# Kernel tuning notes

Hardware: AMD Instinct MI355X
Metric: run time of the kernel (lower is better)

Reference implementation:

```python
import jax, jax.numpy as jnp
import numpy as np

FACTOR = 1.0

def _dct_matrix():
    n = 8
    D = np.zeros((n * n, n * n), dtype=np.float32)
    for u in range(n):
        for v in range(n):
            au = 1.0 / np.sqrt(2.0) if u == 0 else 1.0
            av = 1.0 / np.sqrt(2.0) if v == 0 else 1.0
            alpha = au * av * 0.25
            for x in range(n):
                for y in range(n):
                    D[u * n + v, x * n + y] = alpha * np.cos((2 * x + 1) * u * np.pi / 16) * np.cos((2 * y + 1) * v * np.pi / 16)
    return D

def _y_quant_table():
    t = np.array([[16, 11, 10, 16, 24, 40, 51, 61], [12, 12, 14, 19, 26, 58, 60, 55],
                  [14, 13, 16, 24, 40, 57, 69, 56], [14, 17, 22, 29, 51, 87, 80, 62],
                  [18, 22, 37, 56, 68, 109, 103, 77], [24, 35, 55, 64, 81, 104, 113, 92],
                  [49, 64, 78, 87, 103, 121, 120, 101], [72, 92, 95, 98, 112, 100, 103, 99]],
                 dtype=np.float32).T
    return t

def _c_quant_table():
    t = np.full((8, 8), 99, dtype=np.float32)
    t[:4, :4] = np.array([[17, 18, 24, 47], [18, 21, 26, 66], [24, 26, 56, 99], [47, 66, 99, 99]],
                          dtype=np.float32).T
    return t

_D = jnp.asarray(_dct_matrix())          # [64,64]
_QT = jnp.stack([jnp.asarray(_y_quant_table()),
                 jnp.asarray(_c_quant_table()),
                 jnp.asarray(_c_quant_table())], axis=0) * FACTOR  # [3,8,8]

def setup_inputs() -> dict:
    key = jax.random.key(0)
    image = jax.random.uniform(key, (32, 3, 512, 512), dtype=jnp.float32)
    return {"image": image}

def _diffjpeg(image):
    x = jnp.clip(image, 0.0, 1.0)
    B, C, H, W = x.shape  # H, W multiples of 8 -> no padding branch
    r, g, b = x[:, 0], x[:, 1], x[:, 2]
    y = 0.299 * r + 0.587 * g + 0.114 * b
    cb = (b - y) * 0.564 + 0.5
    cr = (r - y) * 0.713 + 0.5
    ycbcr = jnp.stack([y, cb, cr], axis=1)  # [B,3,H,W]
    # blockify into 8x8 tiles
    nh, nw = H // 8, W // 8
    blocks = ycbcr.reshape(B, C, nh, 8, nw, 8).transpose(0, 1, 2, 4, 3, 5)  # [B,C,nh,nw,8,8]
    flat = blocks.reshape(-1, 64) * 255.0 - 128.0
    dct = flat @ _D.T                      # matmul(D, flat.T).T
    dctb = dct.reshape(B, C, nh, nw, 8, 8)
    qte = _QT[None, :, None, None, :, :]   # [1,3,1,1,8,8]
    q = dctb / qte
    q = q + jax.lax.stop_gradient(jnp.round(q) - q)  # STE rounding
    deq = q * qte
    idct = deq.reshape(-1, 64) @ _D        # matmul(D.T, x.T).T
    idct = (idct + 128.0) / 255.0
    img = idct.reshape(B, C, nh, nw, 8, 8).transpose(0, 1, 2, 4, 3, 5).reshape(B, C, H, W)
    yy, ycb, ycr = img[:, 0], img[:, 1] - 0.5, img[:, 2] - 0.5
    rr = yy + 1.403 * ycr
    gg = yy - 0.714 * ycr - 0.344 * ycb
    bb = yy + 1.773 * ycb
    rgb = jnp.clip(jnp.stack([rr, gg, bb], axis=1), 0.0, 1.0)
    return jnp.clip(rgb, 0.0, 1.0)

def reference(image):
    return _diffjpeg(image)
```

## Files before the change

kernel.cpp:

```cpp
#include <hip/hip_runtime.h>

typedef float f32x2 __attribute__((ext_vector_type(2)));

#define K4 0.353553391f
#define K1 0.490392640f
#define K3 0.415734806f
#define K5 0.277785117f
#define K7 0.097545161f
#define K2 0.461939766f
#define K6 0.191341716f

__device__ __align__(16) const float YQT[64] = {
    16.f, 12.f, 14.f, 14.f,  18.f,  24.f,  49.f,  72.f,
    11.f, 12.f, 13.f, 17.f,  22.f,  35.f,  64.f,  92.f,
    10.f, 14.f, 16.f, 22.f,  37.f,  55.f,  78.f,  95.f,
    16.f, 19.f, 24.f, 29.f,  56.f,  64.f,  87.f,  98.f,
    24.f, 26.f, 40.f, 51.f,  68.f,  81.f, 103.f, 112.f,
    40.f, 58.f, 57.f, 87.f, 109.f, 104.f, 121.f, 100.f,
    51.f, 60.f, 69.f, 80.f, 103.f, 113.f, 120.f, 103.f,
    61.f, 55.f, 56.f, 62.f,  77.f,  92.f, 101.f,  99.f
};
__device__ __align__(16) const float RYQT[64] = {
    1.f/16.f, 1.f/12.f, 1.f/14.f, 1.f/14.f, 1.f/18.f,  1.f/24.f,  1.f/49.f,  1.f/72.f,
    1.f/11.f, 1.f/12.f, 1.f/13.f, 1.f/17.f, 1.f/22.f,  1.f/35.f,  1.f/64.f,  1.f/92.f,
    1.f/10.f, 1.f/14.f, 1.f/16.f, 1.f/22.f, 1.f/37.f,  1.f/55.f,  1.f/78.f,  1.f/95.f,
    1.f/16.f, 1.f/19.f, 1.f/24.f, 1.f/29.f, 1.f/56.f,  1.f/64.f,  1.f/87.f,  1.f/98.f,
    1.f/24.f, 1.f/26.f, 1.f/40.f, 1.f/51.f, 1.f/68.f,  1.f/81.f,  1.f/103.f, 1.f/112.f,
    1.f/40.f, 1.f/58.f, 1.f/57.f, 1.f/87.f, 1.f/109.f, 1.f/104.f, 1.f/121.f, 1.f/100.f,
    1.f/51.f, 1.f/60.f, 1.f/69.f, 1.f/80.f, 1.f/103.f, 1.f/113.f, 1.f/120.f, 1.f/103.f,
    1.f/61.f, 1.f/55.f, 1.f/56.f, 1.f/62.f, 1.f/77.f,  1.f/92.f,  1.f/101.f, 1.f/99.f
};
__device__ __align__(16) const float CQ[64] = {
    17.f, 18.f, 24.f, 47.f, 99.f, 99.f, 99.f, 99.f,
    18.f, 21.f, 26.f, 66.f, 99.f, 99.f, 99.f, 99.f,
    24.f, 26.f, 56.f, 99.f, 99.f, 99.f, 99.f, 99.f,
    47.f, 66.f, 99.f, 99.f, 99.f, 99.f, 99.f, 99.f,
    99.f, 99.f, 99.f, 99.f, 99.f, 99.f, 99.f, 99.f,
    99.f, 99.f, 99.f, 99.f, 99.f, 99.f, 99.f, 99.f,
    99.f, 99.f, 99.f, 99.f, 99.f, 99.f, 99.f, 99.f,
    99.f, 99.f, 99.f, 99.f, 99.f, 99.f, 99.f, 99.f
};
__device__ __align__(16) const float RCQ[64] = {
    1.f/17.f, 1.f/18.f, 1.f/24.f, 1.f/47.f, 1.f/99.f, 1.f/99.f, 1.f/99.f, 1.f/99.f,
    1.f/18.f, 1.f/21.f, 1.f/26.f, 1.f/66.f, 1.f/99.f, 1.f/99.f, 1.f/99.f, 1.f/99.f,
    1.f/24.f, 1.f/26.f, 1.f/56.f, 1.f/99.f, 1.f/99.f, 1.f/99.f, 1.f/99.f, 1.f/99.f,
    1.f/47.f, 1.f/66.f, 1.f/99.f, 1.f/99.f, 1.f/99.f, 1.f/99.f, 1.f/99.f, 1.f/99.f,
    1.f/99.f, 1.f/99.f, 1.f/99.f, 1.f/99.f, 1.f/99.f, 1.f/99.f, 1.f/99.f, 1.f/99.f,
    1.f/99.f, 1.f/99.f, 1.f/99.f, 1.f/99.f, 1.f/99.f, 1.f/99.f, 1.f/99.f, 1.f/99.f,
    1.f/99.f, 1.f/99.f, 1.f/99.f, 1.f/99.f, 1.f/99.f, 1.f/99.f, 1.f/99.f, 1.f/99.f,
    1.f/99.f, 1.f/99.f, 1.f/99.f, 1.f/99.f, 1.f/99.f, 1.f/99.f, 1.f/99.f, 1.f/99.f
};

__device__ __forceinline__ float gfma(float a, float b, float c) { return fmaf(a, b, c); }
__device__ __forceinline__ f32x2 gfma(f32x2 a, f32x2 b, f32x2 c) { return __builtin_elementwise_fma(a, b, c); }
__device__ __forceinline__ f32x2 gfma(float a, f32x2 b, f32x2 c) { return __builtin_elementwise_fma((f32x2){a, a}, b, c); }

__device__ __forceinline__ float clamp01(float x) { return __builtin_amdgcn_fmed3f(x, 0.f, 1.f); }

template <typename T>
__device__ __forceinline__ void dct8(const T x[8], T X[8]) {
    const T a0 = x[0] + x[7], a1 = x[1] + x[6], a2 = x[2] + x[5], a3 = x[3] + x[4];
    const T d0 = x[0] - x[7], d1 = x[1] - x[6], d2 = x[2] - x[5], d3 = x[3] - x[4];
    const T e0 = a0 + a3, e1 = a1 + a2, f0 = a0 - a3, f1 = a1 - a2;
    X[0] = K4 * (e0 + e1);
    X[4] = K4 * (e0 - e1);
    X[2] = gfma(K6, f1, K2 * f0);
    X[6] = gfma(-K2, f1, K6 * f0);
    X[1] = gfma(K7, d3, gfma(K5, d2, gfma(K3, d1, K1 * d0)));
    X[3] = gfma(-K5, d3, gfma(-K1, d2, gfma(-K7, d1, K3 * d0)));
    X[5] = gfma(K3, d3, gfma(K7, d2, gfma(-K1, d1, K5 * d0)));
    X[7] = gfma(-K1, d3, gfma(K3, d2, gfma(-K5, d1, K7 * d0)));
}

template <typename T>
__device__ __forceinline__ void idct8(const T X[8], T x[8]) {
    const T g0 = K4 * (X[0] + X[4]);
    const T g1 = K4 * (X[0] - X[4]);
    const T E0 = gfma(K6, X[6], gfma(K2, X[2], g0));
    const T E1 = gfma(-K2, X[6], gfma(K6, X[2], g1));
    const T E2 = gfma(K2, X[6], gfma(-K6, X[2], g1));
    const T E3 = gfma(-K6, X[6], gfma(-K2, X[2], g0));
    const T O0 = gfma(K7, X[7], gfma(K5, X[5], gfma(K3, X[3], K1 * X[1])));
    const T O1 = gfma(-K5, X[7], gfma(-K1, X[5], gfma(-K7, X[3], K3 * X[1])));
    const T O2 = gfma(K3, X[7], gfma(K7, X[5], gfma(-K1, X[3], K5 * X[1])));
    const T O3 = gfma(-K1, X[7], gfma(K3, X[5], gfma(-K5, X[3], K7 * X[1])));
    x[0] = E0 + O0;  x[7] = E0 - O0;
    x[1] = E1 + O1;  x[6] = E1 - O1;
    x[2] = E2 + O2;  x[5] = E2 - O2;
    x[3] = E3 + O3;  x[4] = E3 - O3;
}

__device__ __forceinline__ f32x2 quant2(f32x2 sv, f32x2 qt, f32x2 rq) {
    const f32x2 q0 = sv * rq;
    const f32x2 e  = gfma(-qt, q0, sv);
    const f32x2 q  = gfma(rq, e, q0);
    const f32x2 n  = {rintf(q.x), rintf(q.y)};
    return n * qt;
}

__device__ __forceinline__ void wave_lds_fence() {
    asm volatile("s_waitcnt lgkmcnt(0)" ::: "memory");
}

#define YW 68
#define CW 70

__global__ __launch_bounds__(256, 8) void diffjpeg_kernel(const float* __restrict__ in,
                                                          float* __restrict__ out)
{
    __shared__ __align__(16) f32x2 lds[4][8][CW];

    const int t  = threadIdx.x;
    const int l  = t & 63;
    const int wv = t >> 6;
    const int b8 = (l >> 3) * 8;
    const int rr = l & 7;

    f32x2 (*plc)[CW] = lds[wv];
    float* ply = (float*)&lds[wv][0][0];

    const int bid  = blockIdx.x;
    const int img  = bid >> 7;
    const int rem  = bid & 127;
    const int trow = rem >> 3;
    const int tcol = rem & 7;
    const size_t HW = (size_t)512 * 512;
    const size_t sbase = (size_t)img * 3 * HW + (size_t)(trow * 32 + wv * 8) * 512 + (size_t)(tcol * 64);
    const float* __restrict__ pin  = in  + sbase + l;
    float* __restrict__       pout = out + sbase + l;

    float rv[8], gv[8], bv[8];
    #pragma unroll
    for (int x = 0; x < 8; ++x) rv[x] = pin[(size_t)x * 512];
    #pragma unroll
    for (int x = 0; x < 8; ++x) gv[x] = pin[HW + (size_t)x * 512];
    #pragma unroll
    for (int x = 0; x < 8; ++x) bv[x] = pin[2 * HW + (size_t)x * 512];

    float yv[8];
    f32x2 cc[8];
    #pragma unroll
    for (int x = 0; x < 8; ++x) {
        const float r = clamp01(rv[x]);
        const float g = clamp01(gv[x]);
        const float b = clamp01(bv[x]);
        const float Y = fmaf(76.245f, r, fmaf(149.685f, g, 29.07f * b));
        yv[x] = Y - 128.f;
        const f32x2 tbr = gfma(255.f, (f32x2){b, r}, (f32x2){-Y, -Y});
        cc[x] = gfma((f32x2){0.564f, 0.713f}, tbr, (f32x2){-0.5f, -0.5f});
    }

    float sy[8];
    {
        float X0[8];
        dct8(yv, X0);
        #pragma unroll
        for (int u = 0; u < 8; ++u) ply[u * YW + l] = X0[u];
        wave_lds_fence();

        {
            const float4* yq4  = (const float4*)&YQT[rr * 8];
            const float4* ryq4 = (const float4*)&RYQT[rr * 8];
            const float4 yqa = yq4[0],  yqb = yq4[1];
            const float4 rya = ryq4[0], ryb = ryq4[1];
            const float yq[8]  = {yqa.x, yqa.y, yqa.z, yqa.w, yqb.x, yqb.y, yqb.z, yqb.w};
            const float ryq[8] = {rya.x, rya.y, rya.z, rya.w, ryb.x, ryb.y, ryb.z, ryb.w};

            float4* rp = (float4*)(ply + rr * YW + b8);
            const float4 a0 = rp[0];
            const float4 a1 = rp[1];
            const float T[8] = {a0.x, a0.y, a0.z, a0.w, a1.x, a1.y, a1.z, a1.w};
            float S[8];
            dct8(T, S);
            float Dq[8];
            #pragma unroll
            for (int i = 0; i < 4; ++i) {
                const f32x2 d = quant2((f32x2){S[2*i], S[2*i+1]},
                                       (f32x2){yq[2*i], yq[2*i+1]},
                                       (f32x2){ryq[2*i], ryq[2*i+1]});
                Dq[2*i] = d.x; Dq[2*i+1] = d.y;
            }
            float o[8];
            idct8(Dq, o);
            rp[0] = make_float4(o[0], o[1], o[2], o[3]);
            rp[1] = make_float4(o[4], o[5], o[6], o[7]);
        }
        wave_lds_fence();

        float Xy[8];
        #pragma unroll
        for (int u = 0; u < 8; ++u) Xy[u] = ply[u * YW + l];
        idct8(Xy, sy);
    }
    wave_lds_fence();

    f32x2 sc[8];
    {
        f32x2 XC[8];
        dct8(cc, XC);
        #pragma unroll
        for (int u = 0; u < 8; ++u) plc[u][l] = XC[u];
        wave_lds_fence();

        {
            const float4* cq4  = (const float4*)&CQ[rr * 8];
            const float4* rcq4 = (const float4*)&RCQ[rr * 8];
            const float4 cqa = cq4[0],  cqb = cq4[1];
            const float4 rca = rcq4[0], rcb4 = rcq4[1];
            const float cq[8]  = {cqa.x, cqa.y, cqa.z, cqa.w, cqb.x, cqb.y, cqb.z, cqb.w};
            const float rcq[8] = {rca.x, rca.y, rca.z, rca.w, rcb4.x, rcb4.y, rcb4.z, rcb4.w};

            float4* rp = (float4*)&plc[rr][b8];
            const float4 p0 = rp[0], p1 = rp[1], p2 = rp[2], p3 = rp[3];
            const f32x2 T[8] = {{p0.x, p0.y}, {p0.z, p0.w}, {p1.x, p1.y}, {p1.z, p1.w},
                                {p2.x, p2.y}, {p2.z, p2.w}, {p3.x, p3.y}, {p3.z, p3.w}};
            f32x2 S[8];
            dct8(T, S);
            f32x2 Dq[8];
            #pragma unroll
            for (int v = 0; v < 8; ++v)
                Dq[v] = quant2(S[v], (f32x2){cq[v], cq[v]}, (f32x2){rcq[v], rcq[v]});
            f32x2 o[8];
            idct8(Dq, o);
            rp[0] = make_float4(o[0].x, o[0].y, o[1].x, o[1].y);
            rp[1] = make_float4(o[2].x, o[2].y, o[3].x, o[3].y);
            rp[2] = make_float4(o[4].x, o[4].y, o[5].x, o[5].y);
            rp[3] = make_float4(o[6].x, o[6].y, o[7].x, o[7].y);
        }
        wave_lds_fence();

        f32x2 Xc[8];
        #pragma unroll
        for (int u = 0; u < 8; ++u) Xc[u] = plc[u][l];
        idct8(Xc, sc);
    }

    {
        constexpr float inv255 = 1.0f / 255.0f;
        constexpr float Kr = 0.504711754f;
        constexpr float Kg = 0.499886280f;
        constexpr float Kb = 0.505437240f;
        #pragma unroll
        for (int x = 0; x < 8; ++x) {
            const float scb = sc[x].x;
            const float scr = sc[x].y;
            const f32x2 inner = gfma((f32x2){1.403f, 1.773f}, (f32x2){scr, scb},
                                     (f32x2){sy[x], sy[x]});
            const f32x2 rb = gfma(inv255, inner, (f32x2){Kr, Kb});
            const float gg = fmaf(inv255, fmaf(-0.714f, scr, fmaf(-0.344f, scb, sy[x])), Kg);
            __builtin_nontemporal_store(clamp01(rb.x), pout + (size_t)x * 512);
            __builtin_nontemporal_store(clamp01(gg),   pout + HW + (size_t)x * 512);
            __builtin_nontemporal_store(clamp01(rb.y), pout + 2 * HW + (size_t)x * 512);
        }
    }
}

extern "C" void kernel_launch(void* const* d_in, const int* in_sizes, int n_in,
                              void* d_out, int out_size, void* d_ws, size_t ws_size,
                              hipStream_t stream) {
    const float* in = (const float*)d_in[0];
    float* out = (float*)d_out;
    const int B = in_sizes[0] / (3 * 512 * 512);
    const int grid = B * 128;
    diffjpeg_kernel<<<grid, 256, 0, stream>>>(in, out);
}
```

Measured before the change: 35.04 us.

## Process two tile rows per block with all loads issued up front

Each block now handles two 32-row tiles, and the global loads for both are issued before any compute begins. This halves the grid and lets the second tile's memory latency hide behind the first tile's DCT work. The explicit s_waitcnt fences are replaced by scheduling barriers, relying on the compiler to insert the LDS waits. More live registers force occupancy down from 8 to 6 blocks per SIMD, and the grid becomes smaller.

```diff
diff --git a/kernel.cpp b/kernel.cpp
--- a/kernel.cpp
+++ b/kernel.cpp
@@ -98,14 +98,12 @@
     return n * qt;
 }
 
-__device__ __forceinline__ void wave_lds_fence() {
-    asm volatile("s_waitcnt lgkmcnt(0)" ::: "memory");
-}
+#define SB() __builtin_amdgcn_sched_barrier(0)
 
 #define YW 68
 #define CW 70
 
-__global__ __launch_bounds__(256, 8) void diffjpeg_kernel(const float* __restrict__ in,
+__global__ __launch_bounds__(256, 6) void diffjpeg_kernel(const float* __restrict__ in,
                                                           float* __restrict__ out)
 {
     __shared__ __align__(16) f32x2 lds[4][8][CW];
@@ -120,45 +118,56 @@
     float* ply = (float*)&lds[wv][0][0];
 
     const int bid  = blockIdx.x;
-    const int img  = bid >> 7;
-    const int rem  = bid & 127;
-    const int trow = rem >> 3;
+    const int img  = bid >> 6;
+    const int rem  = bid & 63;
+    const int brow = rem >> 3;
     const int tcol = rem & 7;
     const size_t HW = (size_t)512 * 512;
-    const size_t sbase = (size_t)img * 3 * HW + (size_t)(trow * 32 + wv * 8) * 512 + (size_t)(tcol * 64);
-    const float* __restrict__ pin  = in  + sbase + l;
-    float* __restrict__       pout = out + sbase + l;
-
-    float rv[8], gv[8], bv[8];
-    #pragma unroll
-    for (int x = 0; x < 8; ++x) rv[x] = pin[(size_t)x * 512];
-    #pragma unroll
-    for (int x = 0; x < 8; ++x) gv[x] = pin[HW + (size_t)x * 512];
-    #pragma unroll
-    for (int x = 0; x < 8; ++x) bv[x] = pin[2 * HW + (size_t)x * 512];
-
-    float yv[8];
-    f32x2 cc[8];
-    #pragma unroll
-    for (int x = 0; x < 8; ++x) {
-        const float r = clamp01(rv[x]);
-        const float g = clamp01(gv[x]);
-        const float b = clamp01(bv[x]);
-        const float Y = fmaf(76.245f, r, fmaf(149.685f, g, 29.07f * b));
-        yv[x] = Y - 128.f;
-        const f32x2 tbr = gfma(255.f, (f32x2){b, r}, (f32x2){-Y, -Y});
-        cc[x] = gfma((f32x2){0.564f, 0.713f}, tbr, (f32x2){-0.5f, -0.5f});
-    }
-
-    float sy[8];
-    {
-        float X0[8];
-        dct8(yv, X0);
+    const size_t sbase = (size_t)img * 3 * HW + (size_t)(brow * 64 + wv * 8) * 512 + (size_t)(tcol * 64);
+    const size_t soff  = (size_t)32 * 512;
+    const float* __restrict__ pinA  = in  + sbase + l;
+    const float* __restrict__ pinB  = pinA + soff;
+    float* __restrict__       poutA = out + sbase + l;
+    float* __restrict__       poutB = poutA + soff;
+
+    float rvA[8], gvA[8], bvA[8], rvB[8], gvB[8], bvB[8];
+    #pragma unroll
+    for (int x = 0; x < 8; ++x) rvA[x] = pinA[(size_t)x * 512];
+    #pragma unroll
+    for (int x = 0; x < 8; ++x) gvA[x] = pinA[HW + (size_t)x * 512];
+    #pragma unroll
+    for (int x = 0; x < 8; ++x) bvA[x] = pinA[2 * HW + (size_t)x * 512];
+    #pragma unroll
+    for (int x = 0; x < 8; ++x) rvB[x] = pinB[(size_t)x * 512];
+    #pragma unroll
+    for (int x = 0; x < 8; ++x) gvB[x] = pinB[HW + (size_t)x * 512];
+    #pragma unroll
+    for (int x = 0; x < 8; ++x) bvB[x] = pinB[2 * HW + (size_t)x * 512];
+    SB();
+
+    auto chain = [&](const float (&rv)[8], const float (&gv)[8], const float (&bv)[8],
+                     float* __restrict__ pout) {
+        float yv[8];
+        f32x2 cc[8];
         #pragma unroll
-        for (int u = 0; u < 8; ++u) ply[u * YW + l] = X0[u];
-        wave_lds_fence();
-
+        for (int x = 0; x < 8; ++x) {
+            const float r = clamp01(rv[x]);
+            const float g = clamp01(gv[x]);
+            const float b = clamp01(bv[x]);
+            const float Y = fmaf(76.245f, r, fmaf(149.685f, g, 29.07f * b));
+            yv[x] = Y - 128.f;
+            const f32x2 tbr = gfma(255.f, (f32x2){b, r}, (f32x2){-Y, -Y});
+            cc[x] = gfma((f32x2){0.564f, 0.713f}, tbr, (f32x2){-0.5f, -0.5f});
+        }
+
+        float sy[8];
         {
+            float X0[8];
+            dct8(yv, X0);
+            #pragma unroll
+            for (int u = 0; u < 8; ++u) ply[u * YW + l] = X0[u];
+            SB();
+
             const float4* yq4  = (const float4*)&YQT[rr * 8];
             const float4* ryq4 = (const float4*)&RYQT[rr * 8];
             const float4 yqa = yq4[0],  yqb = yq4[1];
@@ -184,25 +193,23 @@
             idct8(Dq, o);
             rp[0] = make_float4(o[0], o[1], o[2], o[3]);
             rp[1] = make_float4(o[4], o[5], o[6], o[7]);
-        }
-        wave_lds_fence();
-
-        float Xy[8];
-        #pragma unroll
-        for (int u = 0; u < 8; ++u) Xy[u] = ply[u * YW + l];
-        idct8(Xy, sy);
-    }
-    wave_lds_fence();
-
-    f32x2 sc[8];
-    {
-        f32x2 XC[8];
-        dct8(cc, XC);
-        #pragma unroll
-        for (int u = 0; u < 8; ++u) plc[u][l] = XC[u];
-        wave_lds_fence();
-
+            SB();
+
+            float Xy[8];
+            #pragma unroll
+            for (int u = 0; u < 8; ++u) Xy[u] = ply[u * YW + l];
+            idct8(Xy, sy);
+        }
+        SB();
+
+        f32x2 sc[8];
         {
+            f32x2 XC[8];
+            dct8(cc, XC);
+            #pragma unroll
+            for (int u = 0; u < 8; ++u) plc[u][l] = XC[u];
+            SB();
+
             const float4* cq4  = (const float4*)&CQ[rr * 8];
             const float4* rcq4 = (const float4*)&RCQ[rr * 8];
             const float4 cqa = cq4[0],  cqb = cq4[1];
@@ -226,33 +233,37 @@
             rp[1] = make_float4(o[2].x, o[2].y, o[3].x, o[3].y);
             rp[2] = make_float4(o[4].x, o[4].y, o[5].x, o[5].y);
             rp[3] = make_float4(o[6].x, o[6].y, o[7].x, o[7].y);
-        }
-        wave_lds_fence();
-
-        f32x2 Xc[8];
-        #pragma unroll
-        for (int u = 0; u < 8; ++u) Xc[u] = plc[u][l];
-        idct8(Xc, sc);
-    }
-
-    {
-        constexpr float inv255 = 1.0f / 255.0f;
-        constexpr float Kr = 0.504711754f;
-        constexpr float Kg = 0.499886280f;
-        constexpr float Kb = 0.505437240f;
-        #pragma unroll
-        for (int x = 0; x < 8; ++x) {
-            const float scb = sc[x].x;
-            const float scr = sc[x].y;
-            const f32x2 inner = gfma((f32x2){1.403f, 1.773f}, (f32x2){scr, scb},
-                                     (f32x2){sy[x], sy[x]});
-            const f32x2 rb = gfma(inv255, inner, (f32x2){Kr, Kb});
-            const float gg = fmaf(inv255, fmaf(-0.714f, scr, fmaf(-0.344f, scb, sy[x])), Kg);
-            __builtin_nontemporal_store(clamp01(rb.x), pout + (size_t)x * 512);
-            __builtin_nontemporal_store(clamp01(gg),   pout + HW + (size_t)x * 512);
-            __builtin_nontemporal_store(clamp01(rb.y), pout + 2 * HW + (size_t)x * 512);
-        }
-    }
+            SB();
+
+            f32x2 Xc[8];
+            #pragma unroll
+            for (int u = 0; u < 8; ++u) Xc[u] = plc[u][l];
+            idct8(Xc, sc);
+        }
+
+        {
+            constexpr float inv255 = 1.0f / 255.0f;
+            constexpr float Kr = 0.504711754f;
+            constexpr float Kg = 0.499886280f;
+            constexpr float Kb = 0.505437240f;
+            #pragma unroll
+            for (int x = 0; x < 8; ++x) {
+                const float scb = sc[x].x;
+                const float scr = sc[x].y;
+                const f32x2 inner = gfma((f32x2){1.403f, 1.773f}, (f32x2){scr, scb},
+                                         (f32x2){sy[x], sy[x]});
+                const f32x2 rb = gfma(inv255, inner, (f32x2){Kr, Kb});
+                const float gg = fmaf(inv255, fmaf(-0.714f, scr, fmaf(-0.344f, scb, sy[x])), Kg);
+                __builtin_nontemporal_store(clamp01(rb.x), pout + (size_t)x * 512);
+                __builtin_nontemporal_store(clamp01(gg),   pout + HW + (size_t)x * 512);
+                __builtin_nontemporal_store(clamp01(rb.y), pout + 2 * HW + (size_t)x * 512);
+            }
+        }
+    };
+
+    chain(rvA, gvA, bvA, poutA);
+    SB();
+    chain(rvB, gvB, bvB, poutB);
 }
 
 extern "C" void kernel_launch(void* const* d_in, const int* in_sizes, int n_in,
@@ -261,6 +272,6 @@
     const float* in = (const float*)d_in[0];
     float* out = (float*)d_out;
     const int B = in_sizes[0] / (3 * 512 * 512);
-    const int grid = B * 128;
+    const int grid = B * 64;
     diffjpeg_kernel<<<grid, 256, 0, stream>>>(in, out);
 }
```

Result: slower. 63.08 us (+80.0%).
